# Performance work log

Measured on AMD Instinct MI355X. Metric: run time of the kernel, lower is better.

Reference implementation:

```python
import jax, jax.numpy as jnp
import numpy as np
from math import pi

B, L, S, D, H, M, DK, IND, KS = 8, 3072, 3072, 512, 8, 2, 64, 96, 25


def _linear(x, W, b):
    return x @ W + b


def _moving_avg(x, k):
    # Autoformer-style moving average with edge replication, stride 1.  x: [B, T, D]
    pad = (k - 1) // 2
    xp = jnp.concatenate([jnp.repeat(x[:, :1], pad, axis=1), x,
                          jnp.repeat(x[:, -1:], pad, axis=1)], axis=1)
    c = jnp.cumsum(xp, axis=1)
    c = jnp.concatenate([jnp.zeros_like(c[:, :1]), c], axis=1)
    return (c[:, k:] - c[:, :-k]) / k


def _trend_norm(x, g, b):
    # series_decomp(kernel=25): LayerNorm the seasonal part, add back the trend.
    trend = _moving_avg(x, KS)
    seas = x - trend
    mu = jnp.mean(seas, axis=-1, keepdims=True)
    var = jnp.var(seas, axis=-1, keepdims=True)
    return (seas - mu) * jax.lax.rsqrt(var + 1e-5) * g + b + trend


def _quat_attention(q, k, v, q_om, q_th, k_om, k_th):
    # q: [B,Lq,H,E]; k,v: [B,Sk,H,E]; omegas/thetas: [B,*,H,M]
    Bq, Lq, Hh, E = q.shape
    Sk = k.shape[1]
    Mm = q_om.shape[-1]
    qpos = (jnp.arange(Lq, dtype=q.dtype) / Lq)[None, :, None, None]
    kpos = (jnp.arange(Sk, dtype=q.dtype) / Sk)[None, :, None, None]
    Qa = q_om * qpos + q_th
    Ka = k_om * kpos + k_th
    Qc, Qs = jnp.cos(Qa), jnp.sin(Qa)
    Kc, Ks = jnp.cos(Ka), jnp.sin(Ka)
    q0, q1, q2, q3 = jnp.split(q, 4, axis=-1)
    k0, k1, k2, k3 = jnp.split(k, 4, axis=-1)
    op = lambda a, t: jnp.einsum('blhe,blhm->blhme', a, t)
    Qr = jnp.concatenate([op(q0, Qc) - op(q1, Qs), op(q1, Qc) + op(q0, Qs),
                          op(q2, Qc) + op(q3, Qs), op(q3, Qc) - op(q2, Qs)], axis=-1)
    Kr = jnp.concatenate([op(k0, Kc) - op(k2, Ks), op(k1, Kc) - op(k3, Ks),
                          op(k2, Kc) + op(k0, Ks), op(k3, Kc) + op(k1, Ks)], axis=-1)
    scores = jnp.einsum('blhme,bshme->bhls', Qr, Kr) / Mm
    scale = 1.0 / jnp.sqrt(jnp.asarray(E, q.dtype))
    A = jax.nn.softmax(scale * scores, axis=-1)
    return jnp.einsum('bhls,bshd->blhd', A, v)


def _ltr_layer(p, queries, keys, values):
    Bq, Lq, _ = queries.shape
    Sk = keys.shape[1]
    # kernel_size=1 convs == pointwise linears
    q_om = jax.nn.relu(_linear(queries, p['Wqo'], p['bqo'])).reshape(Bq, Lq, H, M)
    k_om = jax.nn.relu(_linear(keys, p['Wko'], p['bko'])).reshape(Bq, Sk, H, M)
    q_th = (jnp.tanh(_linear(queries, p['Wqt'], p['bqt'])) * pi).reshape(Bq, Lq, H, M)
    k_th = (jnp.tanh(_linear(keys, p['Wkt'], p['bkt'])) * pi).reshape(Bq, Sk, H, M)
    q = _linear(queries, p['Wq'], p['bq']).reshape(Bq, Lq, H, DK)
    k = _linear(keys, p['Wk'], p['bk']).reshape(Bq, Sk, H, DK)
    v = _linear(values, p['Wv'], p['bv']).reshape(Bq, Sk, H, DK)
    out = _quat_attention(q, k, v, q_om, q_th, k_om, k_th).reshape(Bq, Lq, H * DK)
    # D-matrix penalty == first-order difference along sequence
    om_pen = jnp.sum(jnp.diff(q_om, axis=1) ** 2) + jnp.sum(jnp.diff(k_om, axis=1) ** 2)
    th_pen = jnp.sum(q_th ** 2) + jnp.sum(k_th ** 2)
    return _linear(out, p['Wo'], p['bo']), om_pen, th_pen


def setup_inputs() -> dict:
    key = jax.random.key(0)
    ks = iter(jax.random.split(key, 32))
    rn = lambda shape, s=1.0: jax.random.normal(next(ks), shape, jnp.float32) * s
    w = 0.03  # ~1/sqrt(d_model)
    return dict(
        queries=rn((B, L, D)), keys=rn((B, S, D)), values=rn((B, S, D)),
        Wq=rn((2, D, D), w), bq=jnp.zeros((2, D), jnp.float32),
        Wk=rn((2, D, D), w), bk=jnp.zeros((2, D), jnp.float32),
        Wv=rn((2, D, D), w), bv=jnp.zeros((2, D), jnp.float32),
        Wqo=rn((2, D, M * H), w), bqo=jnp.zeros((2, M * H), jnp.float32),
        Wko=rn((2, D, M * H), w), bko=jnp.zeros((2, M * H), jnp.float32),
        Wqt=rn((2, D, M * H), w), bqt=jnp.zeros((2, M * H), jnp.float32),
        Wkt=rn((2, D, M * H), w), bkt=jnp.zeros((2, M * H), jnp.float32),
        Wo=rn((2, D, D), w), bo=jnp.zeros((2, D), jnp.float32),
        I=rn((1, IND, D), w),
        ln_g=jnp.ones((D,), jnp.float32), ln_b=jnp.zeros((D,), jnp.float32),
    )


def reference(queries, keys, values, Wq, bq, Wk, bk, Wv, bv, Wqo, bqo, Wko, bko,
              Wqt, bqt, Wkt, bkt, Wo, bo, I, ln_g, ln_b):
    def lp(i):
        return dict(Wq=Wq[i], bq=bq[i], Wk=Wk[i], bk=bk[i], Wv=Wv[i], bv=bv[i],
                    Wqo=Wqo[i], bqo=bqo[i], Wko=Wko[i], bko=bko[i],
                    Wqt=Wqt[i], bqt=bqt[i], Wkt=Wkt[i], bkt=bkt[i],
                    Wo=Wo[i], bo=bo[i])
    Bq = queries.shape[0]
    inducings = jnp.broadcast_to(I, (Bq, IND, D))
    inducings, om1, th1 = _ltr_layer(lp(0), inducings, keys, values)
    inducings = _trend_norm(inducings, ln_g, ln_b)
    out, om2, th2 = _ltr_layer(lp(1), queries, inducings, inducings)
    return out, om1 + om2, th1 + th2
```

## Files before the change

### kernel.cpp

```cpp
#include <hip/hip_runtime.h>
#include <math.h>

#define PI_F 3.14159265358979323846f

namespace {
constexpr int B_ = 8;
constexpr int L_ = 3072;
constexpr int S_ = 3072;
constexpr int H_ = 8;
constexpr int NF = 544;
constexpr int NSC = 8;
constexpr int SCHUNK = S_ / NSC;
}

typedef __attribute__((ext_vector_type(8))) short bf16x8;
typedef __attribute__((ext_vector_type(4))) float f32x4;

__device__ inline f32x4 mfma16(bf16x8 a, bf16x8 b, f32x4 c) {
  return __builtin_amdgcn_mfma_f32_16x16x32_bf16(a, b, c, 0, 0, 0);
}

__device__ inline ushort f2bf(float f) {
  union { float f; unsigned u; } v;
  v.f = f;
  unsigned r = v.u + 0x7FFFu + ((v.u >> 16) & 1u);
  return (ushort)(r >> 16);
}

__device__ inline void gl_lds16(const void* g, void* l) {
  __builtin_amdgcn_global_load_lds(
      (const __attribute__((address_space(1))) unsigned int*)g,
      (__attribute__((address_space(3))) unsigned int*)l, 16, 0, 0);
}

__global__ void init_pen(float* pen) {
  if (threadIdx.x < 16) pen[threadIdx.x] = 0.f;
}

__global__ void write_pen(const float* __restrict__ pen, float* __restrict__ out) {
  if (threadIdx.x == 0) out[12582912] = pen[0];
  if (threadIdx.x == 1) out[12582913] = pen[1];
}

__global__ void pack_w(const float* __restrict__ Wm, const float* __restrict__ Wo_,
                       const float* __restrict__ Wt, const float* __restrict__ bm,
                       const float* __restrict__ bo_, const float* __restrict__ bt,
                       float* __restrict__ Wcat, float* __restrict__ bcat) {
  int gid = blockIdx.x * 256 + threadIdx.x;
  if (gid < 512 * 544) {
    int k = gid / 544, n = gid % 544;
    float v;
    if (n < 512) v = Wm[(size_t)k * 512 + n];
    else if (n < 528) v = Wo_[k * 16 + (n - 512)];
    else v = Wt[k * 16 + (n - 528)];
    Wcat[gid] = v;
  }
  if (gid < 544) {
    float v;
    if (gid < 512) v = bm[gid];
    else if (gid < 528) v = bo_[gid - 512];
    else v = bt[gid - 528];
    bcat[gid] = v;
  }
}

__global__ void pack_wt_fused(const float* __restrict__ Wm, const float* __restrict__ Wo_,
                              const float* __restrict__ Wt, const float* __restrict__ bm,
                              const float* __restrict__ bo_, const float* __restrict__ bt,
                              ushort* __restrict__ BT, float* __restrict__ bias) {
  int gid = blockIdx.x * 256 + threadIdx.x;
  if (gid < 640 * 512) {
    int n = gid >> 9, k = gid & 511;
    float v = 0.f;
    if (n < 512) v = Wm[(size_t)k * 512 + n];
    else if (n < 528) v = Wo_[k * 16 + (n - 512)];
    else if (n < 544) v = Wt[k * 16 + (n - 528)];
    BT[gid] = f2bf(v);
  }
  if (gid < 544)
    bias[gid] = (gid < 512) ? bm[gid] : (gid < 528 ? bo_[gid - 512] : bt[gid - 528]);
}

__global__ void pack_wt_plain(const float* __restrict__ W, const float* __restrict__ b,
                              ushort* __restrict__ BT, float* __restrict__ bias) {
  int gid = blockIdx.x * 256 + threadIdx.x;
  if (gid < 512 * 512) {
    int n = gid >> 9, k = gid & 511;
    BT[gid] = f2bf(W[(size_t)k * 512 + n]);
  }
  if (gid < 512) bias[gid] = b[gid];
}

__global__ __launch_bounds__(256)
void cast_bf16(const float* __restrict__ src, ushort* __restrict__ dst, int n8) {
  int gid = blockIdx.x * 256 + threadIdx.x;
  if (gid < n8) {
    float4 a = ((const float4*)src)[(size_t)gid * 2];
    float4 b = ((const float4*)src)[(size_t)gid * 2 + 1];
    ushort u[8] = {f2bf(a.x), f2bf(a.y), f2bf(a.z), f2bf(a.w),
                   f2bf(b.x), f2bf(b.y), f2bf(b.z), f2bf(b.w)};
    ((uint4*)dst)[gid] = *(uint4*)u;
  }
}

__global__ __launch_bounds__(256)
void gemm_bf16_mfma(const ushort* __restrict__ A, const ushort* __restrict__ BT,
                    const float* __restrict__ bias, float* __restrict__ C,
                    int ldc, int Nout, int act) {
  __shared__ ushort As[128][32];
  __shared__ ushort Bs[128][32];
  const int tid = threadIdx.x;
  const int wv = tid >> 6, lane = tid & 63, quad = lane >> 4, col = lane & 15;
  const int wm = wv & 1, wn = wv >> 1;
  const int m0 = blockIdx.y * 128, n0 = blockIdx.x * 128;

  const int srow = lane >> 2;
  const int scol = (lane & 3) * 8;

  f32x4 acc[4][4];
#pragma unroll
  for (int i = 0; i < 4; ++i)
#pragma unroll
    for (int j = 0; j < 4; ++j) {
      f32x4 z = {0.f, 0.f, 0.f, 0.f};
      acc[i][j] = z;
    }

  const ushort* Ag = A + (size_t)(m0 + wv * 32) * 512;
  const ushort* Bg = BT + (size_t)(n0 + wv * 32) * 512;

  for (int k0 = 0; k0 < 512; k0 += 32) {
    __syncthreads();
    gl_lds16(Ag + (size_t)srow * 512 + k0 + scol, &As[wv * 32][0]);
    gl_lds16(Ag + (size_t)(srow + 16) * 512 + k0 + scol, &As[wv * 32 + 16][0]);
    gl_lds16(Bg + (size_t)srow * 512 + k0 + scol, &Bs[wv * 32][0]);
    gl_lds16(Bg + (size_t)(srow + 16) * 512 + k0 + scol, &Bs[wv * 32 + 16][0]);
    __syncthreads();
    bf16x8 av[4], bv[4];
#pragma unroll
    for (int mi = 0; mi < 4; ++mi)
      av[mi] = *(const bf16x8*)&As[wm * 64 + mi * 16 + col][quad * 8];
#pragma unroll
    for (int ni = 0; ni < 4; ++ni)
      bv[ni] = *(const bf16x8*)&Bs[wn * 64 + ni * 16 + col][quad * 8];
#pragma unroll
    for (int mi = 0; mi < 4; ++mi)
#pragma unroll
      for (int ni = 0; ni < 4; ++ni)
        acc[mi][ni] = mfma16(av[mi], bv[ni], acc[mi][ni]);
  }

#pragma unroll
  for (int mi = 0; mi < 4; ++mi) {
#pragma unroll
    for (int ni = 0; ni < 4; ++ni) {
      int n = n0 + wn * 64 + ni * 16 + col;
      if (n >= Nout) continue;
      float bs = bias[n];
#pragma unroll
      for (int r = 0; r < 4; ++r) {
        int m = m0 + wm * 64 + mi * 16 + quad * 4 + r;
        float v = acc[mi][ni][r] + bs;
        if (act && n >= 512) v = (n < 528) ? fmaxf(v, 0.f) : tanhf(v) * PI_F;
        C[(size_t)m * ldc + n] = v;
      }
    }
  }
}

__global__ __launch_bounds__(256)
void gemm_k512(const float* __restrict__ A, const float* __restrict__ W,
               const float* __restrict__ bias, float* __restrict__ C,
               int M, int N, int act) {
  __shared__ float As[16][68];
  __shared__ float Ws_[16][68];
  const int tid = threadIdx.x;
  const int tx = tid & 15, ty = tid >> 4;
  const int m0 = blockIdx.y * 64, n0 = blockIdx.x * 64;

  float acc[4][4];
#pragma unroll
  for (int i = 0; i < 4; ++i)
#pragma unroll
    for (int j = 0; j < 4; ++j) acc[i][j] = 0.f;

  const int arow = tid >> 2;
  const int acol4 = (tid & 3) * 4;
  const int wrow = tid >> 4;
  const int wcol4 = (tid & 15) * 4;

  for (int k0 = 0; k0 < 512; k0 += 16) {
    float4 av = make_float4(0.f, 0.f, 0.f, 0.f);
    int gm = m0 + arow;
    if (gm < M) av = *(const float4*)(A + (size_t)gm * 512 + k0 + acol4);
    As[acol4 + 0][arow] = av.x;
    As[acol4 + 1][arow] = av.y;
    As[acol4 + 2][arow] = av.z;
    As[acol4 + 3][arow] = av.w;
    float4 wv;
    int gn = n0 + wcol4;
    if (gn + 3 < N) {
      wv = *(const float4*)(W + (size_t)(k0 + wrow) * N + gn);
    } else {
      float tmp[4] = {0.f, 0.f, 0.f, 0.f};
      for (int u = 0; u < 4; ++u)
        if (gn + u < N) tmp[u] = W[(size_t)(k0 + wrow) * N + gn + u];
      wv = make_float4(tmp[0], tmp[1], tmp[2], tmp[3]);
    }
    *(float4*)&Ws_[wrow][wcol4] = wv;
    __syncthreads();
#pragma unroll
    for (int k = 0; k < 16; ++k) {
      float4 a4 = *(const float4*)&As[k][ty * 4];
      float4 b4 = *(const float4*)&Ws_[k][tx * 4];
      float a[4] = {a4.x, a4.y, a4.z, a4.w};
      float b[4] = {b4.x, b4.y, b4.z, b4.w};
#pragma unroll
      for (int i = 0; i < 4; ++i)
#pragma unroll
        for (int j = 0; j < 4; ++j) acc[i][j] = fmaf(a[i], b[j], acc[i][j]);
    }
    __syncthreads();
  }

#pragma unroll
  for (int i = 0; i < 4; ++i) {
    int gm = m0 + ty * 4 + i;
    if (gm >= M) continue;
#pragma unroll
    for (int j = 0; j < 4; ++j) {
      int gn = n0 + tx * 4 + j;
      if (gn >= N) continue;
      float v = acc[i][j] + bias[gn];
      if (act && gn >= 512) v = (gn < 528) ? fmaxf(v, 0.f) : tanhf(v) * PI_F;
      C[(size_t)gm * N + gn] = v;
    }
  }
}

__global__ __launch_bounds__(256)
void build_qr0(const float* __restrict__ QF0, float* __restrict__ Qr0) {
  const int l = blockIdx.x;
  const float* row = QF0 + (size_t)l * NF;
  __shared__ float2 trig[8][2];
  const int tid = threadIdx.x;
  if (tid < 16) {
    int h = tid >> 1, m = tid & 1;
    float om = row[512 + h * 2 + m], th = row[528 + h * 2 + m];
    float qa = fmaf(om, (float)l / 96.f, th);
    trig[h][m] = make_float2(cosf(qa), sinf(qa));
  }
  __syncthreads();
  for (int idx = tid; idx < 1024; idx += 256) {
    int h = idx >> 7, d = idx & 127;
    int m = d >> 6, r = d & 63, c = r >> 4, e = r & 15;
    float qc = row[h * 64 + c * 16 + e];
    float qp = row[h * 64 + (c ^ 1) * 16 + e];
    float2 tg = trig[h][m];
    float sgn = (c == 0 || c == 3) ? -1.f : 1.f;
    Qr0[((size_t)h * 96 + l) * 128 + d] = fmaf(qc, tg.x, sgn * qp * tg.y);
  }
}

__global__ __launch_bounds__(256)
void build_kr1(const float* __restrict__ KF1, float* __restrict__ Kr1) {
  const int rs = blockIdx.x;
  const int b = rs / 96, s = rs % 96;
  const float* row = KF1 + (size_t)rs * NF;
  __shared__ float2 trig[8][2];
  const int tid = threadIdx.x;
  if (tid < 16) {
    int h = tid >> 1, m = tid & 1;
    float om = row[512 + h * 2 + m], th = row[528 + h * 2 + m];
    float ka = fmaf(om, (float)s / 96.f, th);
    trig[h][m] = make_float2(cosf(ka), sinf(ka));
  }
  __syncthreads();
  for (int idx = tid; idx < 1024; idx += 256) {
    int h = idx >> 7, d = idx & 127;
    int m = d >> 6, r = d & 63, c = r >> 4, e = r & 15;
    float kc = row[h * 64 + c * 16 + e];
    float kp = row[h * 64 + (c ^ 2) * 16 + e];
    float2 tg = trig[h][m];
    float sgn = (c < 2) ? -1.f : 1.f;
    Kr1[(((size_t)(b * 8 + h)) * 96 + s) * 128 + d] = fmaf(kc, tg.x, sgn * kp * tg.y);
  }
}

__global__ __launch_bounds__(256)
void attn0_mfma(const float* __restrict__ KF0, const float* __restrict__ V0,
                const float* __restrict__ Qr0, float* __restrict__ accP,
                float* __restrict__ sumP) {
  const int sc = blockIdx.x, h = blockIdx.y, b = blockIdx.z;
  const int tid = threadIdx.x;
  const int wv = tid >> 6, lane = tid & 63, quad = lane >> 4, col = lane & 15;

  __shared__ __align__(16) ushort Qs[96][136];
  __shared__ __align__(16) ushort Ks[64][136];
  __shared__ __align__(16) ushort Vt[64][72];
  __shared__ __align__(16) ushort Ps[96][72];
  __shared__ float rowsum[96];
  __shared__ float2 trig[64][2];

  const float* Qh = Qr0 + ((size_t)h * 96) * 128;
  for (int idx = tid; idx < 96 * 64; idx += 256) {
    int l = idx >> 6, d2 = (idx & 63) * 2;
    float2 q = *(const float2*)(Qh + (size_t)l * 128 + d2);
    ushort2 u;
    u.x = f2bf(q.x);
    u.y = f2bf(q.y);
    *(ushort2*)&Qs[l][d2] = u;
  }
  if (tid < 96) rowsum[tid] = 0.f;

  f32x4 oacc[6];
#pragma unroll
  for (int i = 0; i < 6; ++i) {
    f32x4 z = {0.f, 0.f, 0.f, 0.f};
    oacc[i] = z;
  }

  const int s0g = sc * SCHUNK;
  for (int t = 0; t < 6; ++t) {
    const int sb = s0g + t * 64;
    __syncthreads();
    if (tid < 128) {
      int s = tid >> 1, m = tid & 1;
      const float* row = KF0 + (size_t)(b * S_ + sb + s) * NF;
      float om = row[512 + h * 2 + m];
      float th = row[528 + h * 2 + m];
      float ka = fmaf(om, (float)(sb + s) * (1.f / (float)S_), th);
      trig[s][m] = make_float2(cosf(ka), sinf(ka));
    }
    __syncthreads();
    for (int idx = tid; idx < 64 * 128; idx += 256) {
      int s = idx >> 7, d = idx & 127;
      int m = d >> 6, r = d & 63, c = r >> 4, e = r & 15;
      const float* row = KF0 + (size_t)(b * S_ + sb + s) * NF + h * 64;
      float kc = row[c * 16 + e];
      float kp = row[(c ^ 2) * 16 + e];
      float2 tg = trig[s][m];
      float sgn = (c < 2) ? -1.f : 1.f;
      Ks[s][d] = f2bf(fmaf(kc, tg.x, sgn * kp * tg.y));
    }
    for (int idx = tid; idx < 64 * 64; idx += 256) {
      int s = idx >> 6, d = idx & 63;
      Vt[d][s] = f2bf(V0[(size_t)(b * S_ + sb + s) * 512 + h * 64 + d]);
    }
    __syncthreads();
    bf16x8 bk[4];
#pragma unroll
    for (int k = 0; k < 4; ++k)
      bk[k] = *(const bf16x8*)&Ks[wv * 16 + col][k * 32 + quad * 8];
    f32x4 sacc[6];
#pragma unroll
    for (int mt = 0; mt < 6; ++mt) {
      f32x4 z = {0.f, 0.f, 0.f, 0.f};
      sacc[mt] = z;
#pragma unroll
      for (int k = 0; k < 4; ++k) {
        bf16x8 a = *(const bf16x8*)&Qs[mt * 16 + col][k * 32 + quad * 8];
        sacc[mt] = mfma16(a, bk[k], sacc[mt]);
      }
    }
#pragma unroll
    for (int mt = 0; mt < 6; ++mt) {
      float pr[4];
#pragma unroll
      for (int r = 0; r < 4; ++r) {
        float p = __expf(sacc[mt][r] * 0.0625f);
        pr[r] = p;
        Ps[mt * 16 + quad * 4 + r][wv * 16 + col] = f2bf(p);
      }
#pragma unroll
      for (int r = 0; r < 4; ++r) {
#pragma unroll
        for (int off = 1; off < 16; off <<= 1) pr[r] += __shfl_xor(pr[r], off);
      }
      if (col == 0) {
#pragma unroll
        for (int r = 0; r < 4; ++r)
          atomicAdd(&rowsum[mt * 16 + quad * 4 + r], pr[r]);
      }
    }
    __syncthreads();
    bf16x8 bv0 = *(const bf16x8*)&Vt[wv * 16 + col][quad * 8];
    bf16x8 bv1 = *(const bf16x8*)&Vt[wv * 16 + col][32 + quad * 8];
#pragma unroll
    for (int mt = 0; mt < 6; ++mt) {
      bf16x8 a0 = *(const bf16x8*)&Ps[mt * 16 + col][quad * 8];
      oacc[mt] = mfma16(a0, bv0, oacc[mt]);
      bf16x8 a1 = *(const bf16x8*)&Ps[mt * 16 + col][32 + quad * 8];
      oacc[mt] = mfma16(a1, bv1, oacc[mt]);
    }
  }
  __syncthreads();
  const size_t pbase = (((size_t)(b * 8 + h)) * NSC + sc) * 96;
#pragma unroll
  for (int mt = 0; mt < 6; ++mt) {
#pragma unroll
    for (int r = 0; r < 4; ++r) {
      int l = mt * 16 + quad * 4 + r;
      accP[(pbase + l) * 64 + wv * 16 + col] = oacc[mt][r];
    }
  }
  if (tid < 96) sumP[pbase + tid] = rowsum[tid];
}

__global__ __launch_bounds__(256)
void attn0_stage2(const float* __restrict__ accP, const float* __restrict__ sumP,
                  float* __restrict__ attn0) {
  const int l = blockIdx.x, b = blockIdx.y;
  const int tid = threadIdx.x;
  for (int e = tid; e < 512; e += 256) {
    int h = e >> 6, d = e & 63;
    size_t base = ((size_t)(b * 8 + h)) * NSC * 96;
    float num = 0.f, den = 0.f;
    for (int scv = 0; scv < NSC; ++scv) {
      size_t pb = base + (size_t)scv * 96 + l;
      num += accP[pb * 64 + d];
      den += sumP[pb];
    }
    attn0[((size_t)(b * 96 + l)) * 512 + e] = num / den;
  }
}

__global__ __launch_bounds__(256)
void trend_norm(const float* __restrict__ y, const float* __restrict__ g,
                const float* __restrict__ be, float* __restrict__ outp) {
  const int t = blockIdx.x, b = blockIdx.y;
  const int tid = threadIdx.x;
  __shared__ float red[256];
  __shared__ float red2[256];
  float seas[2], trend[2];
  float lsum = 0.f, lsum2 = 0.f;
#pragma unroll
  for (int u = 0; u < 2; ++u) {
    int d = tid + u * 256;
    float tr = 0.f;
    for (int j = -12; j <= 12; ++j) {
      int tt = t + j;
      tt = tt < 0 ? 0 : (tt > 95 ? 95 : tt);
      tr += y[((size_t)(b * 96 + tt)) * 512 + d];
    }
    tr *= (1.f / 25.f);
    float x = y[((size_t)(b * 96 + t)) * 512 + d];
    float se = x - tr;
    seas[u] = se;
    trend[u] = tr;
    lsum += se;
    lsum2 += se * se;
  }
  red[tid] = lsum;
  red2[tid] = lsum2;
  __syncthreads();
  for (int off = 128; off > 0; off >>= 1) {
    if (tid < off) {
      red[tid] += red[tid + off];
      red2[tid] += red2[tid + off];
    }
    __syncthreads();
  }
  float mu = red[0] / 512.f;
  float var = red2[0] / 512.f - mu * mu;
  float rs = rsqrtf(var + 1e-5f);
#pragma unroll
  for (int u = 0; u < 2; ++u) {
    int d = tid + u * 256;
    outp[((size_t)(b * 96 + t)) * 512 + d] = (seas[u] - mu) * rs * g[d] + be[d] + trend[u];
  }
}

__global__ __launch_bounds__(256)
void penalty(const float* __restrict__ base, int R, int nb, float mult,
             float* __restrict__ pen) {
  const int tid = threadIdx.x;
  size_t gid = (size_t)blockIdx.x * 256 + tid;
  size_t total = (size_t)nb * R * 16;
  float omv = 0.f, thv = 0.f;
  if (gid < total) {
    int j = (int)(gid & 15);
    size_t row = gid >> 4;
    int s = (int)(row % R);
    const float* r0 = base + row * NF;
    float th = r0[528 + j];
    thv = th * th;
    if (s < R - 1) {
      float d = r0[NF + 512 + j] - r0[512 + j];
      omv = d * d;
    }
  }
  __shared__ float ro[256], rt[256];
  ro[tid] = omv;
  rt[tid] = thv;
  __syncthreads();
  for (int off = 128; off > 0; off >>= 1) {
    if (tid < off) {
      ro[tid] += ro[tid + off];
      rt[tid] += rt[tid + off];
    }
    __syncthreads();
  }
  if (tid == 0) {
    atomicAdd(pen + 0, mult * ro[0]);
    atomicAdd(pen + 1, mult * rt[0]);
  }
}

__global__ __launch_bounds__(256)
void attn1_mfma(const float* __restrict__ QF1, const float* __restrict__ Kr1,
                const float* __restrict__ V1, ushort* __restrict__ attn1) {
  const int lt = blockIdx.x, h = blockIdx.y, b = blockIdx.z;
  const int l0 = lt * 64;
  const int tid = threadIdx.x;
  const int wv = tid >> 6, lane = tid & 63, quad = lane >> 4, col = lane & 15;

  __shared__ __align__(16) ushort Qs[64][136];
  __shared__ __align__(16) ushort Ks[96][136];
  __shared__ __align__(16) ushort Vt[64][104];
  __shared__ __align__(16) ushort Ps[64][104];
  __shared__ float2 trigq[64][2];

  if (tid < 128) {
    int l = tid >> 1, m = tid & 1;
    const float* row = QF1 + (size_t)(b * L_ + l0 + l) * NF;
    float om = row[512 + h * 2 + m];
    float th = row[528 + h * 2 + m];
    float qa = fmaf(om, (float)(l0 + l) * (1.f / (float)L_), th);
    trigq[l][m] = make_float2(cosf(qa), sinf(qa));
  }
  __syncthreads();
  for (int idx = tid; idx < 64 * 128; idx += 256) {
    int l = idx >> 7, d = idx & 127;
    int m = d >> 6, r = d & 63, c = r >> 4, e = r & 15;
    const float* row = QF1 + (size_t)(b * L_ + l0 + l) * NF + h * 64;
    float qc = row[c * 16 + e];
    float qp = row[(c ^ 1) * 16 + e];
    float2 tg = trigq[l][m];
    float sgn = (c == 0 || c == 3) ? -1.f : 1.f;
    Qs[l][d] = f2bf(fmaf(qc, tg.x, sgn * qp * tg.y));
  }
  const float* Krb = Kr1 + (size_t)(b * 8 + h) * 96 * 128;
  for (int idx = tid; idx < 96 * 64; idx += 256) {
    int s = idx >> 6, d2 = (idx & 63) * 2;
    float2 kk = *(const float2*)(Krb + (size_t)s * 128 + d2);
    ushort2 u;
    u.x = f2bf(kk.x);
    u.y = f2bf(kk.y);
    *(ushort2*)&Ks[s][d2] = u;
  }
  for (int idx = tid; idx < 96 * 64; idx += 256) {
    int s = idx >> 6, d = idx & 63;
    Vt[d][s] = f2bf(V1[(size_t)(b * 96 + s) * 512 + h * 64 + d]);
  }
  __syncthreads();

  bf16x8 aq[4];
#pragma unroll
  for (int k = 0; k < 4; ++k)
    aq[k] = *(const bf16x8*)&Qs[wv * 16 + col][k * 32 + quad * 8];
  f32x4 sacc[6];
#pragma unroll
  for (int nt = 0; nt < 6; ++nt) {
    f32x4 z = {0.f, 0.f, 0.f, 0.f};
    sacc[nt] = z;
#pragma unroll
    for (int k = 0; k < 4; ++k) {
      bf16x8 bkf = *(const bf16x8*)&Ks[nt * 16 + col][k * 32 + quad * 8];
      sacc[nt] = mfma16(aq[k], bkf, sacc[nt]);
    }
  }
  float rsum[4] = {0.f, 0.f, 0.f, 0.f};
#pragma unroll
  for (int nt = 0; nt < 6; ++nt) {
#pragma unroll
    for (int r = 0; r < 4; ++r) {
      float p = __expf(sacc[nt][r] * 0.0625f);
      Ps[wv * 16 + quad * 4 + r][nt * 16 + col] = f2bf(p);
      rsum[r] += p;
    }
  }
#pragma unroll
  for (int r = 0; r < 4; ++r) {
#pragma unroll
    for (int off = 1; off < 16; off <<= 1) rsum[r] += __shfl_xor(rsum[r], off);
  }
  __syncthreads();
  bf16x8 ap[3];
#pragma unroll
  for (int kt = 0; kt < 3; ++kt)
    ap[kt] = *(const bf16x8*)&Ps[wv * 16 + col][kt * 32 + quad * 8];
  f32x4 oacc[4];
#pragma unroll
  for (int nt = 0; nt < 4; ++nt) {
    f32x4 z = {0.f, 0.f, 0.f, 0.f};
    oacc[nt] = z;
#pragma unroll
    for (int kt = 0; kt < 3; ++kt) {
      bf16x8 bvf = *(const bf16x8*)&Vt[nt * 16 + col][kt * 32 + quad * 8];
      oacc[nt] = mfma16(ap[kt], bvf, oacc[nt]);
    }
  }
  float inv[4];
#pragma unroll
  for (int r = 0; r < 4; ++r) inv[r] = 1.f / rsum[r];
#pragma unroll
  for (int nt = 0; nt < 4; ++nt) {
#pragma unroll
    for (int r = 0; r < 4; ++r) {
      int l = wv * 16 + quad * 4 + r;
      attn1[(size_t)(b * L_ + l0 + l) * 512 + h * 64 + nt * 16 + col] =
          f2bf(oacc[nt][r] * inv[r]);
    }
  }
}

extern "C" void kernel_launch(void* const* d_in, const int* in_sizes, int n_in,
                              void* d_out, int out_size, void* d_ws, size_t ws_size,
                              hipStream_t stream) {
  (void)in_sizes; (void)n_in; (void)out_size; (void)ws_size;
  const float* queries = (const float*)d_in[0];
  const float* keys = (const float*)d_in[1];
  const float* values = (const float*)d_in[2];
  const float* Wq = (const float*)d_in[3];
  const float* bq = (const float*)d_in[4];
  const float* Wk = (const float*)d_in[5];
  const float* bk = (const float*)d_in[6];
  const float* Wv = (const float*)d_in[7];
  const float* bv = (const float*)d_in[8];
  const float* Wqo = (const float*)d_in[9];
  const float* bqo = (const float*)d_in[10];
  const float* Wko = (const float*)d_in[11];
  const float* bko = (const float*)d_in[12];
  const float* Wqt = (const float*)d_in[13];
  const float* bqt = (const float*)d_in[14];
  const float* Wkt = (const float*)d_in[15];
  const float* bkt = (const float*)d_in[16];
  const float* Wo = (const float*)d_in[17];
  const float* bo = (const float*)d_in[18];
  const float* I = (const float*)d_in[19];
  const float* ln_g = (const float*)d_in[20];
  const float* ln_b = (const float*)d_in[21];
  float* out = (float*)d_out;

  float* ws = (float*)d_ws;
  size_t off = 0;
  auto alloc = [&](size_t n) {
    float* p = ws + off;
    off += (n + 3) & ~(size_t)3;
    return p;
  };
  auto allocU = [&](size_t n) { return (ushort*)alloc((n + 1) / 2); };

  float* WCAT0Q = alloc(512 * 544);
  float* WCAT1K = alloc(512 * 544);
  float* BCAT0Q = alloc(544);
  float* BCAT1K = alloc(544);
  ushort* BT0K = allocU(640 * 512);
  ushort* BT1Q = allocU(640 * 512);
  ushort* BTV0 = allocU(512 * 512);
  ushort* BTO1 = allocU(512 * 512);
  float* B0K = alloc(544);
  float* B1Q = alloc(544);
  float* BV0 = alloc(512);
  float* BO1 = alloc(512);
  float* pen = alloc(16);
  float* QF0 = alloc(96 * 544);
  float* Qr0 = alloc(8 * 96 * 128);
  float* KF0 = alloc((size_t)24576 * 544);
  float* V0 = alloc((size_t)24576 * 512);
  float* attn0 = alloc(768 * 512);
  float* y0 = alloc(768 * 512);
  float* xind = alloc(768 * 512);
  float* KF1 = alloc(768 * 544);
  float* V1 = alloc(768 * 512);
  float* Kr1 = alloc((size_t)64 * 96 * 128);
  float* accP = alloc((size_t)64 * NSC * 96 * 64);
  float* sumP = alloc((size_t)64 * NSC * 96);
  ushort* XB1 = allocU((size_t)24576 * 512);
  ushort* XB2 = allocU((size_t)24576 * 512);
  float* QF1 = KF0;

  init_pen<<<1, 64, 0, stream>>>(pen);
  const int packBlocks = (512 * 544 + 255) / 256;
  pack_w<<<packBlocks, 256, 0, stream>>>(Wq, Wqo, Wqt, bq, bqo, bqt, WCAT0Q, BCAT0Q);
  pack_w<<<packBlocks, 256, 0, stream>>>(Wk + 262144, Wko + 8192, Wkt + 8192,
                                         bk + 512, bko + 16, bkt + 16, WCAT1K, BCAT1K);
  pack_wt_fused<<<(640 * 512 + 255) / 256, 256, 0, stream>>>(
      Wk, Wko, Wkt, bk, bko, bkt, BT0K, B0K);
  pack_wt_fused<<<(640 * 512 + 255) / 256, 256, 0, stream>>>(
      Wq + 262144, Wqo + 8192, Wqt + 8192, bq + 512, bqo + 16, bqt + 16, BT1Q, B1Q);
  pack_wt_plain<<<(512 * 512 + 255) / 256, 256, 0, stream>>>(Wv, bv, BTV0, BV0);
  pack_wt_plain<<<(512 * 512 + 255) / 256, 256, 0, stream>>>(Wo + 262144, bo + 512,
                                                             BTO1, BO1);
  const int castBlocks = (24576 * 512 / 8 + 255) / 256;
  cast_bf16<<<castBlocks, 256, 0, stream>>>(keys, XB1, 24576 * 512 / 8);
  cast_bf16<<<castBlocks, 256, 0, stream>>>(values, XB2, 24576 * 512 / 8);

  gemm_bf16_mfma<<<dim3(5, 192), 256, 0, stream>>>(XB1, BT0K, B0K, KF0, 544, 544, 1);
  gemm_bf16_mfma<<<dim3(4, 192), 256, 0, stream>>>(XB2, BTV0, BV0, V0, 512, 512, 0);
  gemm_k512<<<dim3(9, 2), 256, 0, stream>>>(I, WCAT0Q, BCAT0Q, QF0, 96, 544, 1);
  build_qr0<<<96, 256, 0, stream>>>(QF0, Qr0);
  penalty<<<(96 * 16 + 255) / 256, 256, 0, stream>>>(QF0, 96, 1, 8.f, pen);
  penalty<<<(24576 * 16 + 255) / 256, 256, 0, stream>>>(KF0, 3072, 8, 1.f, pen);
  attn0_mfma<<<dim3(8, 8, 8), 256, 0, stream>>>(KF0, V0, Qr0, accP, sumP);
  attn0_stage2<<<dim3(96, 8), 256, 0, stream>>>(accP, sumP, attn0);
  gemm_k512<<<dim3(8, 12), 256, 0, stream>>>(attn0, Wo, bo, y0, 768, 512, 0);
  trend_norm<<<dim3(96, 8), 256, 0, stream>>>(y0, ln_g, ln_b, xind);

  gemm_k512<<<dim3(9, 12), 256, 0, stream>>>(xind, WCAT1K, BCAT1K, KF1, 768, 544, 1);
  gemm_k512<<<dim3(8, 12), 256, 0, stream>>>(xind, Wv + 262144, bv + 512, V1, 768, 512, 0);
  build_kr1<<<768, 256, 0, stream>>>(KF1, Kr1);
  penalty<<<(768 * 16 + 255) / 256, 256, 0, stream>>>(KF1, 96, 8, 1.f, pen);
  cast_bf16<<<castBlocks, 256, 0, stream>>>(queries, XB1, 24576 * 512 / 8);
  gemm_bf16_mfma<<<dim3(5, 192), 256, 0, stream>>>(XB1, BT1Q, B1Q, QF1, 544, 544, 1);
  penalty<<<(24576 * 16 + 255) / 256, 256, 0, stream>>>(QF1, 3072, 8, 1.f, pen);
  attn1_mfma<<<dim3(48, 8, 8), 256, 0, stream>>>(QF1, Kr1, V1, XB2);
  gemm_bf16_mfma<<<dim3(4, 192), 256, 0, stream>>>(XB2, BTO1, BO1, out, 512, 512, 0);
  write_pen<<<1, 64, 0, stream>>>(pen, out);
}
```

Baseline: 783.5 us.

## Precompute bf16 rotated keys and transposed values for attn0, add XCD swizzle

The rotated keys and transposed values for attention layer 0 are now built once into bf16 buffers by separate kernels. attn0 stages them with 16-byte vector loads instead of doing per-tile trig, gathers and fp32-to-bf16 conversion, and Qr0 is stored directly in bf16. An XCD-aware block-index swizzle is also added to the bf16 GEMM and to attn1 to improve L2 locality across chiplets. The cost is two extra kernel launches and an extra round trip of the K/V intermediates through global memory.

```diff
diff --git a/kernel.cpp b/kernel.cpp
--- a/kernel.cpp
+++ b/kernel.cpp
@@ -31,6 +31,12 @@
   __builtin_amdgcn_global_load_lds(
       (const __attribute__((address_space(1))) unsigned int*)g,
       (__attribute__((address_space(3))) unsigned int*)l, 16, 0, 0);
+}
+
+__device__ inline int xcd_swizzle(int flat, int nwg) {
+  int q = nwg >> 3, r = nwg & 7;
+  int xcd = flat & 7, ix = flat >> 3;
+  return (xcd < r ? xcd * (q + 1) : r * (q + 1) + (xcd - r) * q) + ix;
 }
 
 __global__ void init_pen(float* pen) {
@@ -112,7 +118,12 @@
   const int tid = threadIdx.x;
   const int wv = tid >> 6, lane = tid & 63, quad = lane >> 4, col = lane & 15;
   const int wm = wv & 1, wn = wv >> 1;
-  const int m0 = blockIdx.y * 128, n0 = blockIdx.x * 128;
+
+  const int nwg = gridDim.x * gridDim.y;
+  const int flat = blockIdx.y * gridDim.x + blockIdx.x;
+  const int nf = xcd_swizzle(flat, nwg);
+  const int bx = nf % gridDim.x, by = nf / gridDim.x;
+  const int m0 = by * 128, n0 = bx * 128;
 
   const int srow = lane >> 2;
   const int scol = (lane & 3) * 8;
@@ -239,7 +250,7 @@
 }
 
 __global__ __launch_bounds__(256)
-void build_qr0(const float* __restrict__ QF0, float* __restrict__ Qr0) {
+void build_qr0(const float* __restrict__ QF0, ushort* __restrict__ Qr0bf) {
   const int l = blockIdx.x;
   const float* row = QF0 + (size_t)l * NF;
   __shared__ float2 trig[8][2];
@@ -258,7 +269,54 @@
     float qp = row[h * 64 + (c ^ 1) * 16 + e];
     float2 tg = trig[h][m];
     float sgn = (c == 0 || c == 3) ? -1.f : 1.f;
-    Qr0[((size_t)h * 96 + l) * 128 + d] = fmaf(qc, tg.x, sgn * qp * tg.y);
+    Qr0bf[((size_t)h * 96 + l) * 128 + d] = f2bf(fmaf(qc, tg.x, sgn * qp * tg.y));
+  }
+}
+
+__global__ __launch_bounds__(256)
+void build_kr0(const float* __restrict__ KF0, ushort* __restrict__ Kr0) {
+  const int rs = blockIdx.x;
+  const int b = rs / S_, s = rs - b * S_;
+  const float* row = KF0 + (size_t)rs * NF;
+  __shared__ float2 trig[8][2];
+  const int tid = threadIdx.x;
+  if (tid < 16) {
+    int h = tid >> 1, m = tid & 1;
+    float om = row[512 + h * 2 + m], th = row[528 + h * 2 + m];
+    float ka = fmaf(om, (float)s * (1.f / (float)S_), th);
+    trig[h][m] = make_float2(cosf(ka), sinf(ka));
+  }
+  __syncthreads();
+  for (int idx = tid; idx < 512; idx += 256) {
+    int h = idx >> 6, d = (idx & 63) * 2;
+    int m = d >> 6, r = d & 63, c = r >> 4, e = r & 15;
+    const float* rh = row + h * 64;
+    float2 kc = *(const float2*)(rh + c * 16 + e);
+    float2 kp = *(const float2*)(rh + (c ^ 2) * 16 + e);
+    float2 tg = trig[h][m];
+    float sgn = (c < 2) ? -1.f : 1.f;
+    ushort2 u;
+    u.x = f2bf(fmaf(kc.x, tg.x, sgn * kp.x * tg.y));
+    u.y = f2bf(fmaf(kc.y, tg.x, sgn * kp.y * tg.y));
+    *(ushort2*)&Kr0[(((size_t)(b * 8 + h)) * S_ + s) * 128 + d] = u;
+  }
+}
+
+__global__ __launch_bounds__(256)
+void build_vt0(const float* __restrict__ V0, ushort* __restrict__ Vt0) {
+  const int st = blockIdx.x, h = blockIdx.y, b = blockIdx.z;
+  const int s0 = st * 64;
+  const int tid = threadIdx.x;
+  __shared__ ushort T[64][68];
+  for (int idx = tid; idx < 4096; idx += 256) {
+    int s = idx >> 6, d = idx & 63;
+    T[d][s] = f2bf(V0[((size_t)(b * S_ + s0 + s)) * 512 + h * 64 + d]);
+  }
+  __syncthreads();
+  for (int idx = tid; idx < 2048; idx += 256) {
+    int d = idx >> 5, s2 = (idx & 31) * 2;
+    ushort2 u = *(const ushort2*)&T[d][s2];
+    *(ushort2*)&Vt0[(((size_t)(b * 8 + h)) * 64 + d) * S_ + s0 + s2] = u;
   }
 }
 
@@ -288,8 +346,8 @@
 }
 
 __global__ __launch_bounds__(256)
-void attn0_mfma(const float* __restrict__ KF0, const float* __restrict__ V0,
-                const float* __restrict__ Qr0, float* __restrict__ accP,
+void attn0_mfma(const ushort* __restrict__ Kr0, const ushort* __restrict__ Vt0,
+                const ushort* __restrict__ Qr0bf, float* __restrict__ accP,
                 float* __restrict__ sumP) {
   const int sc = blockIdx.x, h = blockIdx.y, b = blockIdx.z;
   const int tid = threadIdx.x;
@@ -300,16 +358,11 @@
   __shared__ __align__(16) ushort Vt[64][72];
   __shared__ __align__(16) ushort Ps[96][72];
   __shared__ float rowsum[96];
-  __shared__ float2 trig[64][2];
-
-  const float* Qh = Qr0 + ((size_t)h * 96) * 128;
-  for (int idx = tid; idx < 96 * 64; idx += 256) {
-    int l = idx >> 6, d2 = (idx & 63) * 2;
-    float2 q = *(const float2*)(Qh + (size_t)l * 128 + d2);
-    ushort2 u;
-    u.x = f2bf(q.x);
-    u.y = f2bf(q.y);
-    *(ushort2*)&Qs[l][d2] = u;
+
+  const ushort* Qg = Qr0bf + (size_t)h * 96 * 128;
+  for (int idx = tid; idx < 96 * 16; idx += 256) {
+    int l = idx >> 4, c8 = (idx & 15) * 8;
+    *(uint4*)&Qs[l][c8] = *(const uint4*)(Qg + (size_t)l * 128 + c8);
   }
   if (tid < 96) rowsum[tid] = 0.f;
 
@@ -321,31 +374,18 @@
   }
 
   const int s0g = sc * SCHUNK;
+  const ushort* Kb = Kr0 + ((size_t)(b * 8 + h) * S_ + s0g) * 128;
+  const ushort* Vb = Vt0 + ((size_t)(b * 8 + h)) * 64 * S_ + s0g;
+
   for (int t = 0; t < 6; ++t) {
-    const int sb = s0g + t * 64;
-    __syncthreads();
-    if (tid < 128) {
-      int s = tid >> 1, m = tid & 1;
-      const float* row = KF0 + (size_t)(b * S_ + sb + s) * NF;
-      float om = row[512 + h * 2 + m];
-      float th = row[528 + h * 2 + m];
-      float ka = fmaf(om, (float)(sb + s) * (1.f / (float)S_), th);
-      trig[s][m] = make_float2(cosf(ka), sinf(ka));
-    }
-    __syncthreads();
-    for (int idx = tid; idx < 64 * 128; idx += 256) {
-      int s = idx >> 7, d = idx & 127;
-      int m = d >> 6, r = d & 63, c = r >> 4, e = r & 15;
-      const float* row = KF0 + (size_t)(b * S_ + sb + s) * NF + h * 64;
-      float kc = row[c * 16 + e];
-      float kp = row[(c ^ 2) * 16 + e];
-      float2 tg = trig[s][m];
-      float sgn = (c < 2) ? -1.f : 1.f;
-      Ks[s][d] = f2bf(fmaf(kc, tg.x, sgn * kp * tg.y));
-    }
-    for (int idx = tid; idx < 64 * 64; idx += 256) {
-      int s = idx >> 6, d = idx & 63;
-      Vt[d][s] = f2bf(V0[(size_t)(b * S_ + sb + s) * 512 + h * 64 + d]);
+    __syncthreads();
+    for (int idx = tid; idx < 64 * 16; idx += 256) {
+      int s = idx >> 4, c8 = (idx & 15) * 8;
+      *(uint4*)&Ks[s][c8] = *(const uint4*)(Kb + ((size_t)(t * 64 + s)) * 128 + c8);
+    }
+    for (int idx = tid; idx < 64 * 8; idx += 256) {
+      int d = idx >> 3, c8 = (idx & 7) * 8;
+      *(uint4*)&Vt[d][c8] = *(const uint4*)(Vb + (size_t)d * S_ + t * 64 + c8);
     }
     __syncthreads();
     bf16x8 bk[4];
@@ -510,7 +550,12 @@
 __global__ __launch_bounds__(256)
 void attn1_mfma(const float* __restrict__ QF1, const float* __restrict__ Kr1,
                 const float* __restrict__ V1, ushort* __restrict__ attn1) {
-  const int lt = blockIdx.x, h = blockIdx.y, b = blockIdx.z;
+  const int nwg = gridDim.x * gridDim.y * gridDim.z;
+  const int flat = (blockIdx.z * gridDim.y + blockIdx.y) * gridDim.x + blockIdx.x;
+  const int nf = xcd_swizzle(flat, nwg);
+  const int lt = nf % gridDim.x;
+  const int rest = nf / gridDim.x;
+  const int h = rest % gridDim.y, b = rest / gridDim.y;
   const int l0 = lt * 64;
   const int tid = threadIdx.x;
   const int wv = tid >> 6, lane = tid & 63, quad = lane >> 4, col = lane & 15;
@@ -666,7 +711,7 @@
   float* BO1 = alloc(512);
   float* pen = alloc(16);
   float* QF0 = alloc(96 * 544);
-  float* Qr0 = alloc(8 * 96 * 128);
+  ushort* Qr0bf = allocU(8 * 96 * 128);
   float* KF0 = alloc((size_t)24576 * 544);
   float* V0 = alloc((size_t)24576 * 512);
   float* attn0 = alloc(768 * 512);
@@ -679,6 +724,8 @@
   float* sumP = alloc((size_t)64 * NSC * 96);
   ushort* XB1 = allocU((size_t)24576 * 512);
   ushort* XB2 = allocU((size_t)24576 * 512);
+  ushort* Kr0U = XB1;
+  ushort* Vt0U = allocU((size_t)64 * 64 * S_);
   float* QF1 = KF0;
 
   init_pen<<<1, 64, 0, stream>>>(pen);
@@ -700,10 +747,12 @@
   gemm_bf16_mfma<<<dim3(5, 192), 256, 0, stream>>>(XB1, BT0K, B0K, KF0, 544, 544, 1);
   gemm_bf16_mfma<<<dim3(4, 192), 256, 0, stream>>>(XB2, BTV0, BV0, V0, 512, 512, 0);
   gemm_k512<<<dim3(9, 2), 256, 0, stream>>>(I, WCAT0Q, BCAT0Q, QF0, 96, 544, 1);
-  build_qr0<<<96, 256, 0, stream>>>(QF0, Qr0);
+  build_qr0<<<96, 256, 0, stream>>>(QF0, Qr0bf);
   penalty<<<(96 * 16 + 255) / 256, 256, 0, stream>>>(QF0, 96, 1, 8.f, pen);
   penalty<<<(24576 * 16 + 255) / 256, 256, 0, stream>>>(KF0, 3072, 8, 1.f, pen);
-  attn0_mfma<<<dim3(8, 8, 8), 256, 0, stream>>>(KF0, V0, Qr0, accP, sumP);
+  build_kr0<<<24576, 256, 0, stream>>>(KF0, Kr0U);
+  build_vt0<<<dim3(48, 8, 8), 256, 0, stream>>>(V0, Vt0U);
+  attn0_mfma<<<dim3(8, 8, 8), 256, 0, stream>>>(Kr0U, Vt0U, Qr0bf, accP, sumP);
   attn0_stage2<<<dim3(96, 8), 256, 0, stream>>>(accP, sumP, attn0);
   gemm_k512<<<dim3(8, 12), 256, 0, stream>>>(attn0, Wo, bo, y0, 768, 512, 0);
   trend_norm<<<dim3(96, 8), 256, 0, stream>>>(y0, ln_g, ln_b, xind);
```

Result: no change. 772.2 us (-1.4%).
